# Optimization experiments

Hardware: AMD Instinct MI355X
Metric: run time of the kernel (lower is better)

The kernel has to match this reference:

```python
import jax, jax.numpy as jnp
import numpy as np

DIM = 384
PATCH = [(4, 4), (8, 8), (16, 16)]  # (width, height) per channel chunk
B, H, W = 4, 192, 192


def setup_inputs() -> dict:
    key = jax.random.key(0)
    ks = jax.random.split(key, 6)
    c = DIM
    return {
        "rgb": jax.random.normal(ks[0], (B, c, H, W), jnp.float32),
        "fre": jax.random.normal(ks[1], (B, c, H, W), jnp.float32),
        # shared BatchNorm2d (eval-mode affine) applied to both rgb and fre
        "norm_gamma": jnp.ones((c,), jnp.float32),
        "norm_beta": jnp.zeros((c,), jnp.float32),
        "norm_mean": jnp.zeros((c,), jnp.float32),
        "norm_var": jnp.ones((c,), jnp.float32),
        # qv: Conv2d(c, 2c, 1); k: Conv2d(c, c, 1)
        "qv_w": jax.random.normal(ks[2], (2 * c, c), jnp.float32) * 0.02,
        "qv_b": jnp.zeros((2 * c,), jnp.float32),
        "k_w": jax.random.normal(ks[3], (c, c), jnp.float32) * 0.02,
        "k_b": jnp.zeros((c,), jnp.float32),
        # out_conv: Conv2d(c, c, 3, padding=1, bias=False) + BN + LeakyReLU(0.2)
        "oc_w": jax.random.normal(ks[4], (c, c, 3, 3), jnp.float32) * 0.02,
        "oc_gamma": jnp.ones((c,), jnp.float32),
        "oc_beta": jnp.zeros((c,), jnp.float32),
        "oc_mean": jnp.zeros((c,), jnp.float32),
        "oc_var": jnp.ones((c,), jnp.float32),
    }


def _bn(x, g, b, m, v, eps=1e-5):
    scale = g * jax.lax.rsqrt(v + eps)
    return x * scale[None, :, None, None] + (b - m * scale)[None, :, None, None]


def _conv1x1(x, w, b):
    return jnp.einsum('bchw,oc->bohw', x, w) + b[None, :, None, None]


def _win_attn(q, k, v, ww, wh, scale):
    # q,k,v: [b, d, h, w]; window of size (wh x ww)
    b, d, h, w = q.shape
    gh, gw = h // wh, w // ww

    def to_win(t):  # -> [b, gh*gw, wh*ww, d]
        t = t.reshape(b, d, gh, wh, gw, ww).transpose(0, 2, 4, 3, 5, 1)
        return t.reshape(b, gh * gw, wh * ww, d)

    qw, kw, vw = to_win(q), to_win(k), to_win(v)
    attn = jax.nn.softmax((qw * scale) @ kw.swapaxes(-2, -1), axis=-1)
    o = (attn @ vw).reshape(b, gh, gw, wh, ww, d)
    return o.transpose(0, 5, 1, 3, 2, 4).reshape(b, d, h, w)


def reference(rgb, fre, norm_gamma, norm_beta, norm_mean, norm_var,
              qv_w, qv_b, k_w, k_b, oc_w, oc_gamma, oc_beta, oc_mean, oc_var):
    b, c, h, w = rgb.shape
    n = len(PATCH)
    d_k = c // n
    scale = d_k ** (-0.5)

    qv = _conv1x1(_bn(rgb, norm_gamma, norm_beta, norm_mean, norm_var), qv_w, qv_b)
    q, v = qv[:, :c], qv[:, c:]  # reshape(b,2,c,h,w) ordering -> first c = q, next c = v
    k = _conv1x1(_bn(fre, norm_gamma, norm_beta, norm_mean, norm_var), k_w, k_b)

    outs = []
    for i, (ww, wh) in enumerate(PATCH):
        sl = slice(i * d_k, (i + 1) * d_k)
        o = _win_attn(q[:, sl], k[:, sl], v[:, sl], ww, wh, scale) + rgb[:, sl]
        outs.append(o)
    x = jnp.concatenate(outs, axis=1)

    x = jax.lax.conv_general_dilated(x, oc_w, (1, 1), 'SAME',
                                     dimension_numbers=('NCHW', 'OIHW', 'NCHW'))
    x = _bn(x, oc_gamma, oc_beta, oc_mean, oc_var)
    return jnp.where(x >= 0, x, 0.2 * x)  # LeakyReLU(0.2)
```

## Files before the change

### kernel.cpp

```cpp
#include <hip/hip_runtime.h>
#include <stdint.h>

typedef __attribute__((ext_vector_type(8))) short short8;
typedef __attribute__((ext_vector_type(8))) unsigned short ushort8;
typedef __attribute__((ext_vector_type(4))) float f32x4;

#define MFMA(a,b,c) __builtin_amdgcn_mfma_f32_16x16x32_bf16((a),(b),(c),0,0,0)

__device__ __forceinline__ unsigned short f2bf(float f) {
  union { float f; unsigned u; } v; v.f = f;
  unsigned r = v.u + 0x7fffu + ((v.u >> 16) & 1u);
  return (unsigned short)(r >> 16);
}

__device__ __forceinline__ void g2l16(const unsigned short* g, unsigned short* l) {
  __builtin_amdgcn_global_load_lds(
      (const __attribute__((address_space(1))) unsigned int*)(g),
      (__attribute__((address_space(3))) unsigned int*)(l), 16, 0, 0);
}

__device__ __forceinline__ int vswz(int c, int key) {
  return key ^ ((((c >> 3) ^ c) & 7) << 3);
}

__global__ void fold_qvk_kernel(const float* __restrict__ qv_w, const float* __restrict__ qv_b,
                                const float* __restrict__ k_w, const float* __restrict__ k_b,
                                const float* __restrict__ g, const float* __restrict__ be,
                                const float* __restrict__ mu, const float* __restrict__ var,
                                unsigned short* __restrict__ Wq, float* __restrict__ bq,
                                unsigned short* __restrict__ Wk, float* __restrict__ bk) {
  int o = blockIdx.x;
  int t = threadIdx.x;
  bool isq = o < 768;
  int oo = isq ? o : o - 768;
  const float* wrow = isq ? qv_w + (size_t)oo * 384 : k_w + (size_t)oo * 384;
  float mul = (isq && oo < 384) ? 0.08838834764831845f : 1.0f;
  float acc = 0.f;
  for (int c = t; c < 384; c += 128) {
    float sc = g[c] * rsqrtf(var[c] + 1e-5f);
    float sh = be[c] - mu[c] * sc;
    float w = wrow[c];
    acc += w * sh;
    unsigned short wb = f2bf(w * sc * mul);
    if (isq) Wq[(size_t)oo * 384 + c] = wb; else Wk[(size_t)oo * 384 + c] = wb;
  }
#pragma unroll
  for (int m = 1; m < 64; m <<= 1) acc += __shfl_xor(acc, m);
  __shared__ float part[2];
  if ((t & 63) == 0) part[t >> 6] = acc;
  __syncthreads();
  if (t == 0) {
    float b0 = isq ? qv_b[oo] : k_b[oo];
    float bias = (b0 + part[0] + part[1]) * mul;
    if (isq) bq[oo] = bias; else bk[oo] = bias;
  }
}

__global__ void fold_oc_kernel(const float* __restrict__ oc_w,
                               const float* __restrict__ g, const float* __restrict__ be,
                               const float* __restrict__ mu, const float* __restrict__ var,
                               unsigned short* __restrict__ Wc, float* __restrict__ s_oc,
                               float* __restrict__ t_oc) {
  int idx = blockIdx.x * 256 + threadIdx.x;
  if (idx < 384) {
    float sc = g[idx] * rsqrtf(var[idx] + 1e-5f);
    s_oc[idx] = sc;
    t_oc[idx] = be[idx] - mu[idx] * sc;
  }
  if (idx < 384 * 3456) {
    int o = idx / 3456, r = idx % 3456;
    int kq = r / 384, c = r % 384;
    Wc[idx] = f2bf(oc_w[((size_t)o * 384 + c) * 9 + kq]);
  }
}

__launch_bounds__(256)
__global__ void gemm1_kernel(const float* __restrict__ X, const unsigned short* __restrict__ W,
                             const float* __restrict__ bias, unsigned short* __restrict__ Out,
                             int OW, int OT) {
  int bi = blockIdx.x;
  int ot = bi % OT;
  int pt = (bi / OT) % 288;
  int bb = bi / (OT * 288);
  int obase = ot * 128, pbase = pt * 128;
  __shared__ unsigned short As[128 * 40];
  __shared__ unsigned short Bs[128 * 40];
  int tid = threadIdx.x;
  int wv = tid >> 6, lane = tid & 63;
  int l15 = lane & 15, lg = lane >> 4;
  int pw = (wv >> 1) * 64, ow = (wv & 1) * 64;
  f32x4 acc[4][4];
#pragma unroll
  for (int i = 0; i < 4; ++i)
#pragma unroll
    for (int j = 0; j < 4; ++j) acc[i][j] = 0.f;
  const float* Xb = X + (size_t)bb * 384 * 36864;
  int arow = tid >> 1, ahalf = tid & 1;
  int bp = tid & 127, bcg0 = tid >> 7;
  for (int ks = 0; ks < 12; ++ks) {
    int c0 = ks * 32;
    __syncthreads();
    {
      const uint4* s4 = (const uint4*)(W + (size_t)(obase + arow) * 384 + c0 + ahalf * 16);
      uint4 a0 = s4[0], a1 = s4[1];
      uint4* d = (uint4*)&As[arow * 40 + ahalf * 16];
      d[0] = a0; d[1] = a1;
    }
    {
#pragma unroll
      for (int q = 0; q < 2; ++q) {
        int cg = bcg0 + q * 2;
        int cc = c0 + cg * 8;
        const float* src = Xb + (size_t)cc * 36864 + pbase + bp;
        ushort8 t8;
#pragma unroll
        for (int j = 0; j < 8; ++j) t8[j] = f2bf(src[(size_t)j * 36864]);
        *(ushort8*)&Bs[bp * 40 + cg * 8] = t8;
      }
    }
    __syncthreads();
    short8 af[4], bf[4];
#pragma unroll
    for (int f = 0; f < 4; ++f) af[f] = *(const short8*)&Bs[(pw + f * 16 + l15) * 40 + lg * 8];
#pragma unroll
    for (int f = 0; f < 4; ++f) bf[f] = *(const short8*)&As[(ow + f * 16 + l15) * 40 + lg * 8];
#pragma unroll
    for (int fm = 0; fm < 4; ++fm)
#pragma unroll
      for (int fn = 0; fn < 4; ++fn)
        acc[fm][fn] = MFMA(af[fm], bf[fn], acc[fm][fn]);
  }
  unsigned short* Ob = Out + (size_t)bb * 36864 * OW;
#pragma unroll
  for (int fn = 0; fn < 4; ++fn) {
    int o = obase + ow + fn * 16 + l15;
    float bsv = bias[o];
#pragma unroll
    for (int fm = 0; fm < 4; ++fm) {
#pragma unroll
      for (int r = 0; r < 4; ++r) {
        int p = pbase + pw + fm * 16 + lg * 4 + r;
        Ob[(size_t)p * OW + o] = f2bf(acc[fm][fn][r] + bsv);
      }
    }
  }
}

template <int MODE>
__launch_bounds__(256)
__global__ void attn_kernel(const unsigned short* qv, const unsigned short* kx,
                            const float* __restrict__ rgb, unsigned short* xout, int padded) {
  constexpr int GB = MODE * 128;
  constexpr int NKV = (MODE == 2) ? 4 : 1;
  constexpr int NKF = (MODE == 0) ? 1 : 4;
  int bi = blockIdx.x;
  int bb = bi / 576;
  int r5 = bi % 576;
  int tid = threadIdx.x;
  int wv = tid >> 6, lane = tid & 63;
  int l15 = lane & 15, lg = lane >> 4;

  int h0, w0, qtb;
  if (MODE == 0) { int wy = r5 / 12; int wxb = (r5 % 12) * 4; h0 = wy * 4; w0 = wxb * 4; qtb = 0; }
  else if (MODE == 1) { int wy = r5 / 24; int wx = r5 % 24; h0 = wy * 8; w0 = wx * 8; qtb = 0; }
  else { int win = r5 >> 2; int qt = r5 & 3; int wy = win / 12; int wx = win % 12; h0 = wy * 16; w0 = wx * 16; qtb = qt * 64; }

  auto tok2p = [&](int t) -> int {
    if (MODE == 0) { int lw = t >> 4, tt = t & 15; return (h0 + (tt >> 2)) * 192 + w0 + lw * 4 + (tt & 3); }
    else if (MODE == 1) { return (h0 + (t >> 3)) * 192 + w0 + (t & 7); }
    else { return (h0 + (t >> 4)) * 192 + w0 + (t & 15); }
  };

  __shared__ unsigned short Qs[64 * 128];
  __shared__ unsigned short Ks[64 * 128];
  __shared__ unsigned short Vst[128 * 64];
  __shared__ unsigned short Ps[4 * 16 * 72];

  const unsigned short* qvB = qv + (size_t)bb * 36864 * 768;
  const unsigned short* kB = kx + (size_t)bb * 36864 * 384;

  for (int ch = tid; ch < 1024; ch += 256) {
    int tok = ch >> 4, c8 = (ch & 15) << 3;
    int p = tok2p(qtb + tok);
    uint4 v = *(const uint4*)(qvB + (size_t)p * 768 + GB + c8);
    *(uint4*)&Qs[tok * 128 + (c8 ^ ((tok & 7) << 3))] = v;
  }
  __syncthreads();
  short8 qf[4];
  {
    int qrow = wv * 16 + l15;
#pragma unroll
    for (int cs = 0; cs < 4; ++cs)
      qf[cs] = *(const short8*)&Qs[qrow * 128 + ((cs * 32 + lg * 8) ^ ((qrow & 7) << 3))];
  }

  float m[4], s[4];
#pragma unroll
  for (int r = 0; r < 4; ++r) { m[r] = -1e30f; s[r] = 0.f; }
  f32x4 oacc[8];
#pragma unroll
  for (int i = 0; i < 8; ++i) oacc[i] = 0.f;

  for (int kt = 0; kt < NKV; ++kt) {
    __syncthreads();
    for (int ch = tid; ch < 1024; ch += 256) {
      int tok = ch >> 4, c8 = (ch & 15) << 3;
      int p = tok2p(kt * 64 + tok);
      uint4 v = *(const uint4*)(kB + (size_t)p * 384 + GB + c8);
      *(uint4*)&Ks[tok * 128 + (c8 ^ ((tok & 7) << 3))] = v;
    }
    for (int ch = tid; ch < 1024; ch += 256) {
      int key = ch >> 4, c8 = (ch & 15) << 3;
      int p = tok2p(kt * 64 + key);
      ushort8 v = *(const ushort8*)(qvB + (size_t)p * 768 + 384 + GB + c8);
#pragma unroll
      for (int j = 0; j < 8; ++j)
        Vst[(c8 + j) * 64 + vswz(c8 + j, key)] = v[j];
    }
    __syncthreads();

    f32x4 sc[NKF];
#pragma unroll
    for (int kfi = 0; kfi < NKF; ++kfi) {
      int kf = (MODE == 0) ? wv : kfi;
      int krow = kf * 16 + l15;
      f32x4 a; a = 0.f;
#pragma unroll
      for (int cs = 0; cs < 4; ++cs) {
        short8 kfr = *(const short8*)&Ks[krow * 128 + ((cs * 32 + lg * 8) ^ ((krow & 7) << 3))];
        a = MFMA(qf[cs], kfr, a);
      }
      sc[kfi] = a;
    }

    unsigned short* Pw = Ps + wv * (16 * 72);
    float pr[4][NKF];
#pragma unroll
    for (int r = 0; r < 4; ++r) {
      float mx = -1e30f;
#pragma unroll
      for (int kfi = 0; kfi < NKF; ++kfi) mx = fmaxf(mx, sc[kfi][r]);
#pragma unroll
      for (int d = 1; d < 16; d <<= 1) mx = fmaxf(mx, __shfl_xor(mx, d));
      float mn = fmaxf(m[r], mx);
      float f = __expf(m[r] - mn);
      float ls = 0.f;
#pragma unroll
      for (int kfi = 0; kfi < NKF; ++kfi) { float e = __expf(sc[kfi][r] - mn); pr[r][kfi] = e; ls += e; }
#pragma unroll
      for (int d = 1; d < 16; d <<= 1) ls += __shfl_xor(ls, d);
      s[r] = s[r] * f + ls;
      m[r] = mn;
#pragma unroll
      for (int ct = 0; ct < 8; ++ct) oacc[ct][r] *= f;
    }
#pragma unroll
    for (int r = 0; r < 4; ++r) {
      int prow = lg * 4 + r;
#pragma unroll
      for (int kfi = 0; kfi < NKF; ++kfi) {
        int pcol = (MODE == 0) ? l15 : kfi * 16 + l15;
        Pw[prow * 72 + pcol] = f2bf(pr[r][kfi]);
      }
      if (MODE == 0) Pw[prow * 72 + 16 + l15] = 0;
    }
    constexpr int nks = (MODE == 0) ? 1 : 2;
#pragma unroll
    for (int ks = 0; ks < nks; ++ks) {
      short8 pf = *(const short8*)&Pw[l15 * 72 + ks * 32 + lg * 8];
#pragma unroll
      for (int ct = 0; ct < 8; ++ct) {
        int c = ct * 16 + l15;
        short8 vf;
        if (MODE == 0) {
          if (lg < 2) vf = *(const short8*)&Vst[c * 64 + vswz(c, wv * 16 + lg * 8)];
          else vf = 0;
        } else {
          vf = *(const short8*)&Vst[c * 64 + vswz(c, ks * 32 + lg * 8)];
        }
        oacc[ct] = MFMA(pf, vf, oacc[ct]);
      }
    }
  }

  const float* rgbB = rgb + (size_t)bb * 384 * 36864;
  unsigned short* xB = padded ? xout + (size_t)bb * 37636 * 384
                              : xout + (size_t)bb * 36864 * 768;
#pragma unroll
  for (int r = 0; r < 4; ++r) {
    int q64 = wv * 16 + lg * 4 + r;
    int p = tok2p(qtb + q64);
    float inv = 1.0f / s[r];
    size_t rowoff;
    if (padded) {
      int h = p / 192, w = p % 192;
      rowoff = (size_t)((h + 1) * 194 + (w + 1)) * 384;
    } else {
      rowoff = (size_t)p * 768;
    }
#pragma unroll
    for (int ct = 0; ct < 8; ++ct) {
      int c = GB + ct * 16 + l15;
      float val = oacc[ct][r] * inv + rgbB[(size_t)c * 36864 + p];
      xB[rowoff + c] = f2bf(val);
    }
  }
}

__global__ void zero_border_kernel(unsigned short* __restrict__ xpad) {
  int bi = blockIdx.x;
  int bb = bi / 772, i = bi % 772;
  int h, w;
  if (i < 194) { h = 0; w = i; }
  else if (i < 388) { h = 193; w = i - 194; }
  else if (i < 580) { w = 0; h = i - 388 + 1; }
  else { w = 193; h = i - 580 + 1; }
  int t = threadIdx.x;
  if (t < 48) {
    uint4 z = {0, 0, 0, 0};
    uint4* row = (uint4*)(xpad + ((size_t)bb * 37636 + h * 194 + w) * 384);
    row[t] = z;
  }
}

__launch_bounds__(256)
__global__ void conv3p_kernel(const unsigned short* __restrict__ Xp,
                              const unsigned short* __restrict__ Wc,
                              const float* __restrict__ s_oc, const float* __restrict__ t_oc,
                              float* __restrict__ Out) {
  int bid = blockIdx.x;
  int bi = (bid & 7) * 432 + (bid >> 3);
  int pt = bi % 288;
  int ot = (bi / 288) % 3;
  int bb = bi / 864;
  int obase = ot * 128, pbase = pt * 128;
  __shared__ unsigned short As[128 * 32];
  __shared__ unsigned short Bs[128 * 32];
  int tid = threadIdx.x;
  int wv = tid >> 6, lane = tid & 63;
  int l15 = lane & 15, lg = lane >> 4;
  int ow = (wv & 1) * 64, pw = (wv >> 1) * 64;
  f32x4 acc[4][4];
#pragma unroll
  for (int i = 0; i < 4; ++i)
#pragma unroll
    for (int j = 0; j < 4; ++j) acc[i][j] = 0.f;
  int br = lane >> 2;
  int csw = (((lane & 3) ^ ((lane >> 3) & 3)) << 3);
  int p0 = pbase + 32 * wv + br;
  int p1 = p0 + 16;
  int pp0 = (p0 / 192 + 1) * 194 + (p0 % 192 + 1);
  int pp1 = (p1 / 192 + 1) * 194 + (p1 % 192 + 1);
  const unsigned short* Xb = Xp + (size_t)bb * 37636 * 384;
  const unsigned short* Ap0 = Wc + (size_t)(obase + 32 * wv + br) * 3456 + csw;
  const unsigned short* Ap1 = Ap0 + (size_t)16 * 3456;
  const unsigned short* Bp0 = Xb + (size_t)(pp0 - 195) * 384 + csw;
  const unsigned short* Bp1 = Xb + (size_t)(pp1 - 195) * 384 + csw;
  unsigned short* AsB0 = &As[(32 * wv) * 32];
  unsigned short* AsB1 = &As[(32 * wv + 16) * 32];
  unsigned short* BsB0 = &Bs[(32 * wv) * 32];
  unsigned short* BsB1 = &Bs[(32 * wv + 16) * 32];
  int colsw = ((lg ^ ((l15 >> 1) & 3)) << 3);
  for (int seg = 0; seg < 3; ++seg) {
#pragma unroll 4
    for (int k = 0; k < 36; ++k) {
      __syncthreads();
      g2l16(Ap0, AsB0);
      g2l16(Ap1, AsB1);
      g2l16(Bp0, BsB0);
      g2l16(Bp1, BsB1);
      Ap0 += 32; Ap1 += 32; Bp0 += 32; Bp1 += 32;
      __syncthreads();
      short8 af[4], bf2[4];
#pragma unroll
      for (int f = 0; f < 4; ++f) af[f] = *(const short8*)&As[(ow + f * 16 + l15) * 32 + colsw];
#pragma unroll
      for (int f = 0; f < 4; ++f) bf2[f] = *(const short8*)&Bs[(pw + f * 16 + l15) * 32 + colsw];
#pragma unroll
      for (int fm = 0; fm < 4; ++fm)
#pragma unroll
        for (int fn = 0; fn < 4; ++fn)
          acc[fm][fn] = MFMA(af[fm], bf2[fn], acc[fm][fn]);
    }
    Bp0 += 73344; Bp1 += 73344;
  }
  float* Ob = Out + (size_t)bb * 384 * 36864;
#pragma unroll
  for (int fm = 0; fm < 4; ++fm) {
#pragma unroll
    for (int r = 0; r < 4; ++r) {
      int o = obase + ow + fm * 16 + lg * 4 + r;
      float sv = s_oc[o], tv = t_oc[o];
#pragma unroll
      for (int fn = 0; fn < 4; ++fn) {
        int p = pbase + pw + fn * 16 + l15;
        float y = acc[fm][fn][r] * sv + tv;
        Ob[(size_t)o * 36864 + p] = (y >= 0.f) ? y : 0.2f * y;
      }
    }
  }
}

__launch_bounds__(256)
__global__ void conv3_kernel(const unsigned short* __restrict__ X,
                             const unsigned short* __restrict__ Wc,
                             const float* __restrict__ s_oc, const float* __restrict__ t_oc,
                             float* __restrict__ Out) {
  int bi = blockIdx.x;
  int pt = bi % 288;
  int ot = (bi / 288) % 3;
  int bb = bi / 864;
  int obase = ot * 128, pbase = pt * 128;
  __shared__ unsigned short As[128 * 40];
  __shared__ unsigned short Bs[128 * 40];
  int tid = threadIdx.x;
  int wv = tid >> 6, lane = tid & 63;
  int l15 = lane & 15, lg = lane >> 4;
  int ow = (wv & 1) * 64, pw = (wv >> 1) * 64;
  f32x4 acc[4][4];
#pragma unroll
  for (int i = 0; i < 4; ++i)
#pragma unroll
    for (int j = 0; j < 4; ++j) acc[i][j] = 0.f;
  int arow = tid >> 1, ahalf = tid & 1;
  int sp = pbase + arow;
  int sh = sp / 192, sw = sp % 192;
  const unsigned short* Xb = X + (size_t)bb * 36864 * 768;
  for (int ksi = 0; ksi < 108; ++ksi) {
    int kq = ksi / 12;
    int c0 = (ksi % 12) * 32;
    int dh = kq / 3 - 1, dw = kq % 3 - 1;
    __syncthreads();
    {
      const uint4* s4 = (const uint4*)(Wc + (size_t)(obase + arow) * 3456 + kq * 384 + c0 + ahalf * 16);
      uint4 a0 = s4[0], a1 = s4[1];
      uint4* d = (uint4*)&As[arow * 40 + ahalf * 16];
      d[0] = a0; d[1] = a1;
    }
    {
      int hh = sh + dh, ww2 = sw + dw;
      uint4 b0 = {0, 0, 0, 0}, b1 = {0, 0, 0, 0};
      if ((unsigned)hh < 192u && (unsigned)ww2 < 192u) {
        const uint4* s4 = (const uint4*)(Xb + (size_t)(hh * 192 + ww2) * 768 + c0 + ahalf * 16);
        b0 = s4[0]; b1 = s4[1];
      }
      uint4* d = (uint4*)&Bs[arow * 40 + ahalf * 16];
      d[0] = b0; d[1] = b1;
    }
    __syncthreads();
    short8 af[4], bf2[4];
#pragma unroll
    for (int f = 0; f < 4; ++f) af[f] = *(const short8*)&As[(ow + f * 16 + l15) * 40 + lg * 8];
#pragma unroll
    for (int f = 0; f < 4; ++f) bf2[f] = *(const short8*)&Bs[(pw + f * 16 + l15) * 40 + lg * 8];
#pragma unroll
    for (int fm = 0; fm < 4; ++fm)
#pragma unroll
      for (int fn = 0; fn < 4; ++fn)
        acc[fm][fn] = MFMA(af[fm], bf2[fn], acc[fm][fn]);
  }
  float* Ob = Out + (size_t)bb * 384 * 36864;
#pragma unroll
  for (int fm = 0; fm < 4; ++fm) {
#pragma unroll
    for (int r = 0; r < 4; ++r) {
      int o = obase + ow + fm * 16 + lg * 4 + r;
      float sv = s_oc[o], tv = t_oc[o];
#pragma unroll
      for (int fn = 0; fn < 4; ++fn) {
        int p = pbase + pw + fn * 16 + l15;
        float y = acc[fm][fn][r] * sv + tv;
        Ob[(size_t)o * 36864 + p] = (y >= 0.f) ? y : 0.2f * y;
      }
    }
  }
}

extern "C" void kernel_launch(void* const* d_in, const int* in_sizes, int n_in,
                              void* d_out, int out_size, void* d_ws, size_t ws_size,
                              hipStream_t stream) {
  const float* rgb  = (const float*)d_in[0];
  const float* fre  = (const float*)d_in[1];
  const float* ng   = (const float*)d_in[2];
  const float* nb   = (const float*)d_in[3];
  const float* nm   = (const float*)d_in[4];
  const float* nv   = (const float*)d_in[5];
  const float* qv_w = (const float*)d_in[6];
  const float* qv_b = (const float*)d_in[7];
  const float* k_w  = (const float*)d_in[8];
  const float* k_b  = (const float*)d_in[9];
  const float* oc_w = (const float*)d_in[10];
  const float* oc_g = (const float*)d_in[11];
  const float* oc_b = (const float*)d_in[12];
  const float* oc_m = (const float*)d_in[13];
  const float* oc_v = (const float*)d_in[14];

  char* ws = (char*)d_ws;
  const size_t QV_B   = 226492416;
  const size_t K_B    = 113246208;
  const size_t XPAD_B = 115617792;
  size_t off = 0;
  unsigned short* qvbuf = (unsigned short*)(ws + off); off += QV_B;
  unsigned short* kbuf  = (unsigned short*)(ws + off); off += K_B;
  size_t xpad_off = off;
  bool fast = (ws_size >= xpad_off + XPAD_B + 4 * 1024 * 1024);
  unsigned short* xpad = (unsigned short*)(ws + xpad_off);
  if (fast) off += XPAD_B;
  unsigned short* Wq = (unsigned short*)(ws + off); off += 589824;
  unsigned short* Wk = (unsigned short*)(ws + off); off += 294912;
  unsigned short* Wc = (unsigned short*)(ws + off); off += 2654208;
  float* bq  = (float*)(ws + off); off += 3072;
  float* bk  = (float*)(ws + off); off += 1536;
  float* soc = (float*)(ws + off); off += 1536;
  float* toc = (float*)(ws + off); off += 1536;
  float* out = (float*)d_out;

  if (fast) zero_border_kernel<<<dim3(4 * 772), dim3(64), 0, stream>>>(xpad);
  fold_qvk_kernel<<<dim3(1152), dim3(128), 0, stream>>>(qv_w, qv_b, k_w, k_b, ng, nb, nm, nv, Wq, bq, Wk, bk);
  fold_oc_kernel<<<dim3(5184), dim3(256), 0, stream>>>(oc_w, oc_g, oc_b, oc_m, oc_v, Wc, soc, toc);
  gemm1_kernel<<<dim3(4 * 288 * 6), dim3(256), 0, stream>>>(rgb, Wq, bq, qvbuf, 768, 6);
  gemm1_kernel<<<dim3(4 * 288 * 3), dim3(256), 0, stream>>>(fre, Wk, bk, kbuf, 384, 3);
  unsigned short* xdst = fast ? xpad : qvbuf;
  int padded = fast ? 1 : 0;
  attn_kernel<0><<<dim3(2304), dim3(256), 0, stream>>>(qvbuf, kbuf, rgb, xdst, padded);
  attn_kernel<1><<<dim3(2304), dim3(256), 0, stream>>>(qvbuf, kbuf, rgb, xdst, padded);
  attn_kernel<2><<<dim3(2304), dim3(256), 0, stream>>>(qvbuf, kbuf, rgb, xdst, padded);
  if (fast)
    conv3p_kernel<<<dim3(4 * 3 * 288), dim3(256), 0, stream>>>(xpad, Wc, soc, toc, out);
  else
    conv3_kernel<<<dim3(4 * 3 * 288), dim3(256), 0, stream>>>(qvbuf, Wc, soc, toc, out);
}
```

Baseline: 1.401 ms.

## Double-buffer conv3x3 LDS tiles and widen block to 512 threads

The padded 3x3 conv kernel now uses 512-thread blocks covering 128 output channels by 256 pixels, halving the grid. Global-to-LDS loads go through two LDS buffers, so the next k-slice is prefetched while MFMAs run on the current one, with explicit vmcnt waits and raw s_barrier. This is meant to hide load latency behind compute and to halve how often each weight tile is reloaded. The cost is more LDS per block, which can lower occupancy, and the hand-managed waitcnt depends on the exact number of outstanding loads.

```diff
diff --git a/kernel.cpp b/kernel.cpp
--- a/kernel.cpp
+++ b/kernel.cpp
@@ -323,77 +323,84 @@
   }
 }
 
-__launch_bounds__(256)
-__global__ void conv3p_kernel(const unsigned short* __restrict__ Xp,
+__launch_bounds__(512)
+__global__ void conv3d_kernel(const unsigned short* __restrict__ Xp,
                               const unsigned short* __restrict__ Wc,
                               const float* __restrict__ s_oc, const float* __restrict__ t_oc,
                               float* __restrict__ Out) {
   int bid = blockIdx.x;
-  int bi = (bid & 7) * 432 + (bid >> 3);
-  int pt = bi % 288;
-  int ot = (bi / 288) % 3;
-  int bb = bi / 864;
-  int obase = ot * 128, pbase = pt * 128;
-  __shared__ unsigned short As[128 * 32];
-  __shared__ unsigned short Bs[128 * 32];
+  int bi = (bid & 7) * 216 + (bid >> 3);
+  int pt = bi % 144;
+  int ot = (bi / 144) % 3;
+  int bb = bi / 432;
+  int obase = ot * 128, pbase = pt * 256;
+  __shared__ unsigned short Ws2[2][128 * 32];
+  __shared__ unsigned short Xs2[2][256 * 32];
   int tid = threadIdx.x;
   int wv = tid >> 6, lane = tid & 63;
   int l15 = lane & 15, lg = lane >> 4;
-  int ow = (wv & 1) * 64, pw = (wv >> 1) * 64;
+  int wc = wv & 1, wr = wv >> 1;
   f32x4 acc[4][4];
 #pragma unroll
   for (int i = 0; i < 4; ++i)
 #pragma unroll
     for (int j = 0; j < 4; ++j) acc[i][j] = 0.f;
-  int br = lane >> 2;
+  int rl = lane >> 2;
   int csw = (((lane & 3) ^ ((lane >> 3) & 3)) << 3);
-  int p0 = pbase + 32 * wv + br;
+  const unsigned short* Ap = Wc + (size_t)(obase + 16 * wv + rl) * 3456 + csw;
+  int p0 = pbase + 32 * wv + rl;
   int p1 = p0 + 16;
-  int pp0 = (p0 / 192 + 1) * 194 + (p0 % 192 + 1);
-  int pp1 = (p1 / 192 + 1) * 194 + (p1 % 192 + 1);
   const unsigned short* Xb = Xp + (size_t)bb * 37636 * 384;
-  const unsigned short* Ap0 = Wc + (size_t)(obase + 32 * wv + br) * 3456 + csw;
-  const unsigned short* Ap1 = Ap0 + (size_t)16 * 3456;
-  const unsigned short* Bp0 = Xb + (size_t)(pp0 - 195) * 384 + csw;
-  const unsigned short* Bp1 = Xb + (size_t)(pp1 - 195) * 384 + csw;
-  unsigned short* AsB0 = &As[(32 * wv) * 32];
-  unsigned short* AsB1 = &As[(32 * wv + 16) * 32];
-  unsigned short* BsB0 = &Bs[(32 * wv) * 32];
-  unsigned short* BsB1 = &Bs[(32 * wv + 16) * 32];
+  const unsigned short* Bp0 = Xb + (size_t)((p0 / 192 + 1) * 194 + (p0 % 192 + 1) - 195) * 384 + csw;
+  const unsigned short* Bp1 = Xb + (size_t)((p1 / 192 + 1) * 194 + (p1 % 192 + 1) - 195) * 384 + csw;
   int colsw = ((lg ^ ((l15 >> 1) & 3)) << 3);
-  for (int seg = 0; seg < 3; ++seg) {
-#pragma unroll 4
-    for (int k = 0; k < 36; ++k) {
-      __syncthreads();
-      g2l16(Ap0, AsB0);
-      g2l16(Ap1, AsB1);
-      g2l16(Bp0, BsB0);
-      g2l16(Bp1, BsB1);
-      Ap0 += 32; Ap1 += 32; Bp0 += 32; Bp1 += 32;
-      __syncthreads();
-      short8 af[4], bf2[4];
-#pragma unroll
-      for (int f = 0; f < 4; ++f) af[f] = *(const short8*)&As[(ow + f * 16 + l15) * 32 + colsw];
-#pragma unroll
-      for (int f = 0; f < 4; ++f) bf2[f] = *(const short8*)&Bs[(pw + f * 16 + l15) * 32 + colsw];
-#pragma unroll
-      for (int fm = 0; fm < 4; ++fm)
-#pragma unroll
-        for (int fn = 0; fn < 4; ++fn)
-          acc[fm][fn] = MFMA(af[fm], bf2[fn], acc[fm][fn]);
-    }
-    Bp0 += 73344; Bp1 += 73344;
+  unsigned short* WsW = &Ws2[0][(16 * wv) * 32];
+  unsigned short* XsW0 = &Xs2[0][(32 * wv) * 32];
+  unsigned short* XsW1 = &Xs2[0][(32 * wv + 16) * 32];
+  const int WBUF = 128 * 32, XBUF = 256 * 32;
+  g2l16(Ap, WsW);
+  g2l16(Bp0, XsW0);
+  g2l16(Bp1, XsW1);
+  Ap += 32; Bp0 += 32; Bp1 += 32;
+  for (int t = 0; t < 108; ++t) {
+    int cur = t & 1, nxt = cur ^ 1;
+    if (t < 107) {
+      g2l16(Ap, WsW + nxt * WBUF);
+      g2l16(Bp0, XsW0 + nxt * XBUF);
+      g2l16(Bp1, XsW1 + nxt * XBUF);
+      Ap += 32; Bp0 += 32; Bp1 += 32;
+      if (t == 34 || t == 70) { Bp0 += 73344; Bp1 += 73344; }
+      asm volatile("s_waitcnt vmcnt(3)" ::: "memory");
+    } else {
+      asm volatile("s_waitcnt vmcnt(0)" ::: "memory");
+    }
+    __builtin_amdgcn_s_barrier();
+    __builtin_amdgcn_sched_barrier(0);
+    const unsigned short* Wt = &Ws2[cur][0];
+    const unsigned short* Xt = &Xs2[cur][0];
+    short8 af[4], bf2[4];
+#pragma unroll
+    for (int f = 0; f < 4; ++f) af[f] = *(const short8*)&Wt[(wc * 64 + f * 16 + l15) * 32 + colsw];
+#pragma unroll
+    for (int f = 0; f < 4; ++f) bf2[f] = *(const short8*)&Xt[(wr * 64 + f * 16 + l15) * 32 + colsw];
+#pragma unroll
+    for (int fm = 0; fm < 4; ++fm)
+#pragma unroll
+      for (int fn = 0; fn < 4; ++fn)
+        acc[fm][fn] = MFMA(af[fm], bf2[fn], acc[fm][fn]);
+    __builtin_amdgcn_s_barrier();
+    __builtin_amdgcn_sched_barrier(0);
   }
   float* Ob = Out + (size_t)bb * 384 * 36864;
 #pragma unroll
   for (int fm = 0; fm < 4; ++fm) {
 #pragma unroll
     for (int r = 0; r < 4; ++r) {
-      int o = obase + ow + fm * 16 + lg * 4 + r;
+      int o = obase + wc * 64 + fm * 16 + lg * 4 + r;
       float sv = s_oc[o], tv = t_oc[o];
 #pragma unroll
       for (int fn = 0; fn < 4; ++fn) {
-        int p = pbase + pw + fn * 16 + l15;
+        int p = pbase + wr * 64 + fn * 16 + l15;
         float y = acc[fm][fn][r] * sv + tv;
         Ob[(size_t)o * 36864 + p] = (y >= 0.f) ? y : 0.2f * y;
       }
@@ -526,7 +533,7 @@
   attn_kernel<1><<<dim3(2304), dim3(256), 0, stream>>>(qvbuf, kbuf, rgb, xdst, padded);
   attn_kernel<2><<<dim3(2304), dim3(256), 0, stream>>>(qvbuf, kbuf, rgb, xdst, padded);
   if (fast)
-    conv3p_kernel<<<dim3(4 * 3 * 288), dim3(256), 0, stream>>>(xpad, Wc, soc, toc, out);
+    conv3d_kernel<<<dim3(1728), dim3(512), 0, stream>>>(xpad, Wc, soc, toc, out);
   else
     conv3_kernel<<<dim3(4 * 3 * 288), dim3(256), 0, stream>>>(qvbuf, Wc, soc, toc, out);
 }
```

New measurement: 1.324 ms. 5.5% less time.
